# Performance work log

Hardware: AMD Instinct MI355X
Metric: run time of the kernel (lower is better)

Reference implementation:

```python
import jax, jax.numpy as jnp
import numpy as np

N, HW, L = 16, 3136, 64
C_IN, C_OUT, D = 256, 512, 256


def setup_inputs() -> dict:
    key = jax.random.key(0)
    ks = jax.random.split(key, 8)
    # xavier-normal-ish scale for weights
    def xav(k, shape):
        fan_in, fan_out = shape[1], shape[0]
        std = (2.0 / (fan_in + fan_out)) ** 0.5
        return jax.random.normal(k, shape, dtype=jnp.float32) * std
    return {
        "x": jax.random.normal(ks[0], (N, HW, C_IN), dtype=jnp.float32),
        "t": jax.random.normal(ks[1], (N, L, D), dtype=jnp.float32),
        "W1": xav(ks[2], (D, C_IN)),      # linear1 weight (out,in), no bias
        "W2": xav(ks[3], (D, D)),         # linear2 weight, no bias
        "W3": xav(ks[4], (C_OUT, D)),     # linear3 weight
        "b3": jnp.zeros((C_OUT,), dtype=jnp.float32),
        "Wd": xav(ks[5], (C_OUT, C_IN)),  # downsample weight
        "bd": jnp.zeros((C_OUT,), dtype=jnp.float32),
    }


def reference(x, t, W1, W2, W3, b3, Wd, bd):
    # x: (N, HW, C_in), t: (N, L, D)
    x_q = jnp.einsum("npc,dc->npd", x, W1)          # (N, HW, D)
    t_q = jnp.einsum("nld,ed->nle", t, W2)          # (N, L, D)
    a = jnp.einsum("npd,nld->npl", x_q, t_q)        # unscaled QK^T (N, HW, L)
    a = jax.nn.softmax(a, axis=2)
    t3 = jnp.einsum("nld,od->nlo", t, W3) + b3      # (N, L, C_out)
    av = jnp.einsum("npl,nlo->npo", a, t3)          # (N, HW, C_out)
    x_ds = jnp.einsum("npc,oc->npo", x, Wd) + bd    # downsample residual
    return x_ds + av
```

## Files before the change

kernel.cpp:

```cpp
#include <hip/hip_runtime.h>


typedef unsigned short u16;
using half8 = __attribute__((ext_vector_type(8))) _Float16;
using f32x4 = __attribute__((ext_vector_type(4))) float;

__device__ __forceinline__ u16 f2h(float f) {
  _Float16 h = (_Float16)f;
  union { _Float16 h; u16 u; } cv; cv.h = h;
  return cv.u;
}

__device__ __forceinline__ f32x4 mfma16(half8 a, half8 b, f32x4 c) {
  return __builtin_amdgcn_mfma_f32_16x16x32_f16(a, b, c, 0, 0, 0);
}

__global__ __launch_bounds__(256) void prep_kernel(
    const float* __restrict__ W1, const float* __restrict__ W2,
    const float* __restrict__ W3, const float* __restrict__ Wd,
    const float* __restrict__ t,
    u16* __restrict__ W3f, u16* __restrict__ Wdf, u16* __restrict__ tf,
    u16* __restrict__ Gtf) {
  int b = blockIdx.x, k = threadIdx.x;
  if (b < 2048) {
    const float* src; u16* dst; int row;
    if (b < 512)       { src = W3; dst = W3f; row = b; }
    else if (b < 1024) { src = Wd; dst = Wdf; row = b - 512; }
    else               { src = t;  dst = tf;  row = b - 1024; }
    float v = src[(size_t)row*256 + k];
    int flat = ((row >> 4)*8 + (k >> 5))*512 + ((k >> 3) & 3)*128 + (row & 15)*8 + (k & 7);
    dst[flat] = f2h(v);
  } else {
    int c = b - 2048;
    float g = 0.f;
    #pragma unroll 16
    for (int d = 0; d < 256; ++d)
      g = fmaf(W1[d*256 + c], W2[d*256 + k], g);
    int flat = ((c >> 4)*8 + (k >> 5))*512 + ((k >> 3) & 3)*128 + (c & 15)*8 + (k & 7);
    Gtf[flat] = f2h(g);
  }
}

__global__ __launch_bounds__(256) void mt_t3_kernel(
    const u16* __restrict__ tf, const u16* __restrict__ Gtf,
    const u16* __restrict__ W3f, const float* __restrict__ b3,
    u16* __restrict__ mtf, u16* __restrict__ t3f) {
  const int tid = threadIdx.x, w = tid >> 6, lane = tid & 63;
  const int quad = lane >> 4, l16 = lane & 15;
  const int b = blockIdx.x;

  if (b < 64) {
    const int n = b >> 2, eb = b & 3;
    const int gc = eb*4 + w;
    f32x4 acc[4];
    #pragma unroll
    for (int mt = 0; mt < 4; ++mt) acc[mt] = (f32x4){0.f, 0.f, 0.f, 0.f};
    #pragma unroll
    for (int kc = 0; kc < 8; ++kc) {
      half8 bf = *(const half8*)(Gtf + (gc*8 + kc)*512 + lane*8);
      #pragma unroll
      for (int mt = 0; mt < 4; ++mt) {
        half8 a = *(const half8*)(tf + ((n*4 + mt)*8 + kc)*512 + lane*8);
        acc[mt] = mfma16(a, bf, acc[mt]);
      }
    }
    #pragma unroll
    for (int mt = 0; mt < 4; ++mt)
      #pragma unroll
      for (int r = 0; r < 4; ++r) {
        int flat = ((n*4 + mt)*8 + eb*2 + (w >> 1))*512
                 + ((w & 1)*2 + (l16 >> 3))*128 + (quad*4 + r)*8 + (l16 & 7);
        mtf[flat] = f2h(acc[mt][r]);
      }
  } else {
    const int b2 = b - 64;
    const int n = b2 >> 3, ob = b2 & 7;
    const int gW3 = ob*4 + w;
    f32x4 acc[4];
    #pragma unroll
    for (int nt = 0; nt < 4; ++nt) acc[nt] = (f32x4){0.f, 0.f, 0.f, 0.f};
    #pragma unroll
    for (int kc = 0; kc < 8; ++kc) {
      half8 a = *(const half8*)(W3f + (gW3*8 + kc)*512 + lane*8);
      #pragma unroll
      for (int nt = 0; nt < 4; ++nt) {
        half8 bf = *(const half8*)(tf + ((n*4 + nt)*8 + kc)*512 + lane*8);
        acc[nt] = mfma16(a, bf, acc[nt]);
      }
    }
    #pragma unroll
    for (int nt = 0; nt < 4; ++nt)
      #pragma unroll
      for (int r = 0; r < 4; ++r) {
        int o = ob*64 + w*16 + quad*4 + r;
        int flat = ((n*32 + ob*4 + w)*2 + (nt >> 1))*512
                 + ((nt & 1)*2 + (l16 >> 3))*128 + (quad*4 + r)*8 + (l16 & 7);
        t3f[flat] = f2h(acc[nt][r] + b3[o]);
      }
  }
}

__global__ __launch_bounds__(512, 4) void main_kernel(
    const float* __restrict__ x, const u16* __restrict__ Wdf,
    const u16* __restrict__ mtf, const u16* __restrict__ t3f,
    const float* __restrict__ bd, float* __restrict__ out) {
  __shared__ __attribute__((aligned(16))) char smem[62464];
  u16* xs = (u16*)smem;
  u16* aw = (u16*)(smem + 33792);
  float* parts = (float*)(smem + 43008);
  float* scb = (float*)(smem + 44032);

  const int bid = blockIdx.x;
  const int n  = bid / 49;
  const int pt = bid - n*49;
  const int m0 = pt * 64;
  const int tid = threadIdx.x, w = tid >> 6, lane = tid & 63;
  const int quad = lane >> 4, l16 = lane & 15;
  const int rg = w & 3;
  const int lp = w >> 2;

  float bias[4];
  #pragma unroll
  for (int ot = 0; ot < 4; ++ot) bias[ot] = bd[w*64 + ot*16 + l16];

  {
    const float4* xg = (const float4*)(x + (size_t)(n*3136 + m0)*256);
    #pragma unroll
    for (int it = 0; it < 8; ++it) {
      int idx = it*512 + tid;
      int r = idx >> 6, c4 = idx & 63;
      float4 v = xg[idx];
      ushort4 u;
      u.x = f2h(v.x); u.y = f2h(v.y); u.z = f2h(v.z); u.w = f2h(v.w);
      *(ushort4*)(&xs[r*264 + c4*4]) = u;
    }
  }
  __syncthreads();

  f32x4 acc2[2];
  acc2[0] = (f32x4){0.f, 0.f, 0.f, 0.f};
  acc2[1] = (f32x4){0.f, 0.f, 0.f, 0.f};
  #pragma unroll
  for (int kc = 0; kc < 8; ++kc) {
    half8 a = *(const half8*)(&xs[(rg*16 + l16)*264 + kc*32 + quad*8]);
    #pragma unroll
    for (int j = 0; j < 2; ++j) {
      half8 bf = *(const half8*)(mtf + ((size_t)(n*4 + lp*2 + j)*8 + kc)*512 + lane*8);
      acc2[j] = mfma16(a, bf, acc2[j]);
    }
  }

  float mx_[4], ps_[4], e0_[4], e1_[4];
  #pragma unroll
  for (int r = 0; r < 4; ++r) {
    float s0 = acc2[0][r], s1 = acc2[1][r];
    float mx = fmaxf(s0, s1);
    #pragma unroll
    for (int off = 8; off >= 1; off >>= 1) mx = fmaxf(mx, __shfl_xor(mx, off, 64));
    float e0 = __expf(s0 - mx), e1 = __expf(s1 - mx);
    float ps = e0 + e1;
    #pragma unroll
    for (int off = 8; off >= 1; off >>= 1) ps += __shfl_xor(ps, off, 64);
    mx_[r] = mx; ps_[r] = ps; e0_[r] = e0; e1_[r] = e1;
    if (l16 == 0) {
      int row = rg*16 + quad*4 + r;
      parts[(row*2 + lp)*2]     = mx;
      parts[(row*2 + lp)*2 + 1] = ps;
    }
  }
  __syncthreads();

  #pragma unroll
  for (int r = 0; r < 4; ++r) {
    int row = rg*16 + quad*4 + r;
    float mxo = parts[(row*2 + (1 - lp))*2];
    float pso = parts[(row*2 + (1 - lp))*2 + 1];
    float g  = fmaxf(mx_[r], mxo);
    float sA = __expf(mx_[r] - g), sB = __expf(mxo - g);
    float inv = 1.0f / (ps_[r]*sA + pso*sB);
    float scl = sA * inv;
    aw[row*72 + (lp*2)*16 + l16]     = f2h(e0_[r]*scl);
    aw[row*72 + (lp*2 + 1)*16 + l16] = f2h(e1_[r]*scl);
  }
  __syncthreads();

  float* sc = scb + w*576;
  f32x4 acc[4][2];

  #pragma unroll
  for (int mt = 0; mt < 4; ++mt)
    #pragma unroll
    for (int ot = 0; ot < 2; ++ot) acc[mt][ot] = (f32x4){0.f, 0.f, 0.f, 0.f};
  #pragma unroll
  for (int kc = 0; kc < 8; ++kc) {
    half8 a[4];
    #pragma unroll
    for (int mt = 0; mt < 4; ++mt)
      a[mt] = *(const half8*)(&xs[(mt*16 + l16)*264 + kc*32 + quad*8]);
    #pragma unroll
    for (int ot = 0; ot < 2; ++ot) {
      half8 bf = *(const half8*)(Wdf + ((size_t)(w*4 + ot)*8 + kc)*512 + lane*8);
      #pragma unroll
      for (int mt = 0; mt < 4; ++mt) acc[mt][ot] = mfma16(a[mt], bf, acc[mt][ot]);
    }
  }
  #pragma unroll
  for (int kc3 = 0; kc3 < 2; ++kc3) {
    half8 a3[4];
    #pragma unroll
    for (int mt = 0; mt < 4; ++mt)
      a3[mt] = *(const half8*)(&aw[(mt*16 + l16)*72 + kc3*32 + quad*8]);
    #pragma unroll
    for (int ot = 0; ot < 2; ++ot) {
      half8 bf = *(const half8*)(t3f + ((size_t)(n*32 + w*4 + ot)*2 + kc3)*512 + lane*8);
      #pragma unroll
      for (int mt = 0; mt < 4; ++mt) acc[mt][ot] = mfma16(a3[mt], bf, acc[mt][ot]);
    }
  }
  #pragma unroll
  for (int mt = 0; mt < 4; ++mt) {
    #pragma unroll
    for (int ot = 0; ot < 2; ++ot)
      #pragma unroll
      for (int r = 0; r < 4; ++r)
        sc[(quad*4 + r)*36 + ot*16 + l16] = acc[mt][ot][r] + bias[ot];
    #pragma unroll
    for (int shot = 0; shot < 2; ++shot) {
      int row = shot*8 + (lane >> 3);
      float4 v = *(float4*)&sc[row*36 + (lane & 7)*4];
      *(float4*)&out[(size_t)(n*3136 + m0 + mt*16 + row)*512 + w*64 + (lane & 7)*4] = v;
    }
  }

  #pragma unroll
  for (int mt = 0; mt < 4; ++mt)
    #pragma unroll
    for (int ot = 0; ot < 2; ++ot) acc[mt][ot] = (f32x4){0.f, 0.f, 0.f, 0.f};
  #pragma unroll
  for (int kc = 0; kc < 8; ++kc) {
    half8 a[4];
    #pragma unroll
    for (int mt = 0; mt < 4; ++mt)
      a[mt] = *(const half8*)(&xs[(mt*16 + l16)*264 + kc*32 + quad*8]);
    #pragma unroll
    for (int ot = 0; ot < 2; ++ot) {
      half8 bf = *(const half8*)(Wdf + ((size_t)(w*4 + 2 + ot)*8 + kc)*512 + lane*8);
      #pragma unroll
      for (int mt = 0; mt < 4; ++mt) acc[mt][ot] = mfma16(a[mt], bf, acc[mt][ot]);
    }
  }
  #pragma unroll
  for (int kc3 = 0; kc3 < 2; ++kc3) {
    half8 a3[4];
    #pragma unroll
    for (int mt = 0; mt < 4; ++mt)
      a3[mt] = *(const half8*)(&aw[(mt*16 + l16)*72 + kc3*32 + quad*8]);
    #pragma unroll
    for (int ot = 0; ot < 2; ++ot) {
      half8 bf = *(const half8*)(t3f + ((size_t)(n*32 + w*4 + 2 + ot)*2 + kc3)*512 + lane*8);
      #pragma unroll
      for (int mt = 0; mt < 4; ++mt) acc[mt][ot] = mfma16(a3[mt], bf, acc[mt][ot]);
    }
  }
  #pragma unroll
  for (int mt = 0; mt < 4; ++mt) {
    #pragma unroll
    for (int ot = 0; ot < 2; ++ot)
      #pragma unroll
      for (int r = 0; r < 4; ++r)
        sc[(quad*4 + r)*36 + ot*16 + l16] = acc[mt][ot][r] + bias[2 + ot];
    #pragma unroll
    for (int shot = 0; shot < 2; ++shot) {
      int row = shot*8 + (lane >> 3);
      float4 v = *(float4*)&sc[row*36 + (lane & 7)*4];
      *(float4*)&out[(size_t)(n*3136 + m0 + mt*16 + row)*512 + w*64 + 32 + (lane & 7)*4] = v;
    }
  }
}

extern "C" void kernel_launch(void* const* d_in, const int* in_sizes, int n_in,
                              void* d_out, int out_size, void* d_ws, size_t ws_size,
                              hipStream_t stream) {
  const float* x  = (const float*)d_in[0];
  const float* t  = (const float*)d_in[1];
  const float* W1 = (const float*)d_in[2];
  const float* W2 = (const float*)d_in[3];
  const float* W3 = (const float*)d_in[4];
  const float* b3 = (const float*)d_in[5];
  const float* Wd = (const float*)d_in[6];
  const float* bd = (const float*)d_in[7];
  float* out = (float*)d_out;

  char* ws = (char*)d_ws;
  u16* W3f = (u16*)(ws + 0);
  u16* Wdf = (u16*)(ws + 262144);
  u16* tf  = (u16*)(ws + 524288);
  u16* Gtf = (u16*)(ws + 1048576);
  u16* mtf = (u16*)(ws + 1179648);
  u16* t3f = (u16*)(ws + 1703936);

  hipLaunchKernelGGL(prep_kernel, dim3(2304), dim3(256), 0, stream,
                     W1, W2, W3, Wd, t, W3f, Wdf, tf, Gtf);
  hipLaunchKernelGGL(mt_t3_kernel, dim3(192), dim3(256), 0, stream,
                     tf, Gtf, W3f, b3, mtf, t3f);
  hipLaunchKernelGGL(main_kernel, dim3(784), dim3(512), 0, stream,
                     x, Wdf, mtf, t3f, bd, out);
}
```

Baseline: 203.0 us.

## Make main kernel persistent with double-buffered x tile prefetch

The main kernel becomes persistent: it launches 256 blocks, one per CU, and each block loops over 3 or 4 of the 784 tiles. The next tile's x is loaded into registers early and converted into a second LDS buffer at the end of each iteration, so global loads overlap with MFMA work. This removes the wave-quantization tail and the per-block prologue. In exchange the LDS footprint grows, occupancy drops to 2 blocks per SM in launch bounds, and the 32 prefetch registers raise register pressure.

```diff
diff --git a/kernel.cpp b/kernel.cpp
--- a/kernel.cpp
+++ b/kernel.cpp
@@ -100,20 +100,19 @@
   }
 }
 
-__global__ __launch_bounds__(512, 4) void main_kernel(
+__global__ __launch_bounds__(512, 2) void main_kernel(
     const float* __restrict__ x, const u16* __restrict__ Wdf,
     const u16* __restrict__ mtf, const u16* __restrict__ t3f,
     const float* __restrict__ bd, float* __restrict__ out) {
-  __shared__ __attribute__((aligned(16))) char smem[62464];
-  u16* xs = (u16*)smem;
-  u16* aw = (u16*)(smem + 33792);
-  float* parts = (float*)(smem + 43008);
-  float* scb = (float*)(smem + 44032);
-
-  const int bid = blockIdx.x;
-  const int n  = bid / 49;
-  const int pt = bid - n*49;
-  const int m0 = pt * 64;
+  __shared__ __attribute__((aligned(16))) char smem[96256];
+  u16* xs0 = (u16*)smem;
+  u16* xs1 = (u16*)(smem + 33792);
+  u16* aw  = (u16*)(smem + 67584);
+  float* parts = (float*)(smem + 76800);
+  float* scb = (float*)(smem + 77824);
+
+  const int b = blockIdx.x;
+  const int NT = (b < 16) ? 4 : 3;
   const int tid = threadIdx.x, w = tid >> 6, lane = tid & 63;
   const int quad = lane >> 4, l16 = lane & 15;
   const int rg = w & 3;
@@ -123,158 +122,193 @@
   #pragma unroll
   for (int ot = 0; ot < 4; ++ot) bias[ot] = bd[w*64 + ot*16 + l16];
 
+  float* sc = scb + w*576;
+
+  float4 vx[8];
   {
-    const float4* xg = (const float4*)(x + (size_t)(n*3136 + m0)*256);
+    int n0 = b / 49, m00 = (b - n0*49)*64;
+    const float4* xg = (const float4*)(x + (size_t)(n0*3136 + m00)*256);
+    #pragma unroll
+    for (int it = 0; it < 8; ++it) vx[it] = xg[it*512 + tid];
     #pragma unroll
     for (int it = 0; it < 8; ++it) {
       int idx = it*512 + tid;
       int r = idx >> 6, c4 = idx & 63;
-      float4 v = xg[idx];
       ushort4 u;
-      u.x = f2h(v.x); u.y = f2h(v.y); u.z = f2h(v.z); u.w = f2h(v.w);
-      *(ushort4*)(&xs[r*264 + c4*4]) = u;
+      u.x = f2h(vx[it].x); u.y = f2h(vx[it].y);
+      u.z = f2h(vx[it].z); u.w = f2h(vx[it].w);
+      *(ushort4*)(&xs0[r*264 + c4*4]) = u;
     }
   }
   __syncthreads();
 
-  f32x4 acc2[2];
-  acc2[0] = (f32x4){0.f, 0.f, 0.f, 0.f};
-  acc2[1] = (f32x4){0.f, 0.f, 0.f, 0.f};
-  #pragma unroll
-  for (int kc = 0; kc < 8; ++kc) {
-    half8 a = *(const half8*)(&xs[(rg*16 + l16)*264 + kc*32 + quad*8]);
-    #pragma unroll
-    for (int j = 0; j < 2; ++j) {
-      half8 bf = *(const half8*)(mtf + ((size_t)(n*4 + lp*2 + j)*8 + kc)*512 + lane*8);
-      acc2[j] = mfma16(a, bf, acc2[j]);
-    }
-  }
-
-  float mx_[4], ps_[4], e0_[4], e1_[4];
-  #pragma unroll
-  for (int r = 0; r < 4; ++r) {
-    float s0 = acc2[0][r], s1 = acc2[1][r];
-    float mx = fmaxf(s0, s1);
-    #pragma unroll
-    for (int off = 8; off >= 1; off >>= 1) mx = fmaxf(mx, __shfl_xor(mx, off, 64));
-    float e0 = __expf(s0 - mx), e1 = __expf(s1 - mx);
-    float ps = e0 + e1;
-    #pragma unroll
-    for (int off = 8; off >= 1; off >>= 1) ps += __shfl_xor(ps, off, 64);
-    mx_[r] = mx; ps_[r] = ps; e0_[r] = e0; e1_[r] = e1;
-    if (l16 == 0) {
+  for (int ti = 0; ti < NT; ++ti) {
+    u16* xc = (ti & 1) ? xs1 : xs0;
+    u16* xn = (ti & 1) ? xs0 : xs1;
+    const int tile = b + ti*256;
+    const int n = tile / 49;
+    const int m0 = (tile - n*49)*64;
+    const bool more = (ti + 1 < NT);
+
+    if (more) {
+      int tile2 = b + (ti + 1)*256;
+      int n2 = tile2 / 49, m02 = (tile2 - n2*49)*64;
+      const float4* xg2 = (const float4*)(x + (size_t)(n2*3136 + m02)*256);
+      #pragma unroll
+      for (int it = 0; it < 8; ++it) vx[it] = xg2[it*512 + tid];
+    }
+
+    f32x4 acc2[2];
+    acc2[0] = (f32x4){0.f, 0.f, 0.f, 0.f};
+    acc2[1] = (f32x4){0.f, 0.f, 0.f, 0.f};
+    #pragma unroll
+    for (int kc = 0; kc < 8; ++kc) {
+      half8 a = *(const half8*)(&xc[(rg*16 + l16)*264 + kc*32 + quad*8]);
+      #pragma unroll
+      for (int j = 0; j < 2; ++j) {
+        half8 bf = *(const half8*)(mtf + ((size_t)(n*4 + lp*2 + j)*8 + kc)*512 + lane*8);
+        acc2[j] = mfma16(a, bf, acc2[j]);
+      }
+    }
+
+    float mx_[4], ps_[4], e0_[4], e1_[4];
+    #pragma unroll
+    for (int r = 0; r < 4; ++r) {
+      float s0 = acc2[0][r], s1 = acc2[1][r];
+      float mx = fmaxf(s0, s1);
+      #pragma unroll
+      for (int off = 8; off >= 1; off >>= 1) mx = fmaxf(mx, __shfl_xor(mx, off, 64));
+      float e0 = __expf(s0 - mx), e1 = __expf(s1 - mx);
+      float ps = e0 + e1;
+      #pragma unroll
+      for (int off = 8; off >= 1; off >>= 1) ps += __shfl_xor(ps, off, 64);
+      mx_[r] = mx; ps_[r] = ps; e0_[r] = e0; e1_[r] = e1;
+      if (l16 == 0) {
+        int row = rg*16 + quad*4 + r;
+        parts[(row*2 + lp)*2]     = mx;
+        parts[(row*2 + lp)*2 + 1] = ps;
+      }
+    }
+    __syncthreads();
+
+    #pragma unroll
+    for (int r = 0; r < 4; ++r) {
       int row = rg*16 + quad*4 + r;
-      parts[(row*2 + lp)*2]     = mx;
-      parts[(row*2 + lp)*2 + 1] = ps;
-    }
-  }
-  __syncthreads();
-
-  #pragma unroll
-  for (int r = 0; r < 4; ++r) {
-    int row = rg*16 + quad*4 + r;
-    float mxo = parts[(row*2 + (1 - lp))*2];
-    float pso = parts[(row*2 + (1 - lp))*2 + 1];
-    float g  = fmaxf(mx_[r], mxo);
-    float sA = __expf(mx_[r] - g), sB = __expf(mxo - g);
-    float inv = 1.0f / (ps_[r]*sA + pso*sB);
-    float scl = sA * inv;
-    aw[row*72 + (lp*2)*16 + l16]     = f2h(e0_[r]*scl);
-    aw[row*72 + (lp*2 + 1)*16 + l16] = f2h(e1_[r]*scl);
-  }
-  __syncthreads();
-
-  float* sc = scb + w*576;
-  f32x4 acc[4][2];
-
-  #pragma unroll
-  for (int mt = 0; mt < 4; ++mt)
-    #pragma unroll
-    for (int ot = 0; ot < 2; ++ot) acc[mt][ot] = (f32x4){0.f, 0.f, 0.f, 0.f};
-  #pragma unroll
-  for (int kc = 0; kc < 8; ++kc) {
-    half8 a[4];
+      float mxo = parts[(row*2 + (1 - lp))*2];
+      float pso = parts[(row*2 + (1 - lp))*2 + 1];
+      float g  = fmaxf(mx_[r], mxo);
+      float sA = __expf(mx_[r] - g), sB = __expf(mxo - g);
+      float inv = 1.0f / (ps_[r]*sA + pso*sB);
+      float scl = sA * inv;
+      aw[row*72 + (lp*2)*16 + l16]     = f2h(e0_[r]*scl);
+      aw[row*72 + (lp*2 + 1)*16 + l16] = f2h(e1_[r]*scl);
+    }
+    __syncthreads();
+
+    f32x4 acc[4][2];
+
     #pragma unroll
     for (int mt = 0; mt < 4; ++mt)
-      a[mt] = *(const half8*)(&xs[(mt*16 + l16)*264 + kc*32 + quad*8]);
-    #pragma unroll
-    for (int ot = 0; ot < 2; ++ot) {
-      half8 bf = *(const half8*)(Wdf + ((size_t)(w*4 + ot)*8 + kc)*512 + lane*8);
-      #pragma unroll
-      for (int mt = 0; mt < 4; ++mt) acc[mt][ot] = mfma16(a[mt], bf, acc[mt][ot]);
-    }
-  }
-  #pragma unroll
-  for (int kc3 = 0; kc3 < 2; ++kc3) {
-    half8 a3[4];
+      #pragma unroll
+      for (int ot = 0; ot < 2; ++ot) acc[mt][ot] = (f32x4){0.f, 0.f, 0.f, 0.f};
+    #pragma unroll
+    for (int kc = 0; kc < 8; ++kc) {
+      half8 a[4];
+      #pragma unroll
+      for (int mt = 0; mt < 4; ++mt)
+        a[mt] = *(const half8*)(&xc[(mt*16 + l16)*264 + kc*32 + quad*8]);
+      #pragma unroll
+      for (int ot = 0; ot < 2; ++ot) {
+        half8 bf = *(const half8*)(Wdf + ((size_t)(w*4 + ot)*8 + kc)*512 + lane*8);
+        #pragma unroll
+        for (int mt = 0; mt < 4; ++mt) acc[mt][ot] = mfma16(a[mt], bf, acc[mt][ot]);
+      }
+    }
+    #pragma unroll
+    for (int kc3 = 0; kc3 < 2; ++kc3) {
+      half8 a3[4];
+      #pragma unroll
+      for (int mt = 0; mt < 4; ++mt)
+        a3[mt] = *(const half8*)(&aw[(mt*16 + l16)*72 + kc3*32 + quad*8]);
+      #pragma unroll
+      for (int ot = 0; ot < 2; ++ot) {
+        half8 bf = *(const half8*)(t3f + ((size_t)(n*32 + w*4 + ot)*2 + kc3)*512 + lane*8);
+        #pragma unroll
+        for (int mt = 0; mt < 4; ++mt) acc[mt][ot] = mfma16(a3[mt], bf, acc[mt][ot]);
+      }
+    }
+    #pragma unroll
+    for (int mt = 0; mt < 4; ++mt) {
+      #pragma unroll
+      for (int ot = 0; ot < 2; ++ot)
+        #pragma unroll
+        for (int r = 0; r < 4; ++r)
+          sc[(quad*4 + r)*36 + ot*16 + l16] = acc[mt][ot][r] + bias[ot];
+      #pragma unroll
+      for (int shot = 0; shot < 2; ++shot) {
+        int row = shot*8 + (lane >> 3);
+        float4 v = *(float4*)&sc[row*36 + (lane & 7)*4];
+        *(float4*)&out[(size_t)(n*3136 + m0 + mt*16 + row)*512 + w*64 + (lane & 7)*4] = v;
+      }
+    }
+
     #pragma unroll
     for (int mt = 0; mt < 4; ++mt)
-      a3[mt] = *(const half8*)(&aw[(mt*16 + l16)*72 + kc3*32 + quad*8]);
-    #pragma unroll
-    for (int ot = 0; ot < 2; ++ot) {
-      half8 bf = *(const half8*)(t3f + ((size_t)(n*32 + w*4 + ot)*2 + kc3)*512 + lane*8);
-      #pragma unroll
-      for (int mt = 0; mt < 4; ++mt) acc[mt][ot] = mfma16(a3[mt], bf, acc[mt][ot]);
-    }
-  }
-  #pragma unroll
-  for (int mt = 0; mt < 4; ++mt) {
-    #pragma unroll
-    for (int ot = 0; ot < 2; ++ot)
-      #pragma unroll
-      for (int r = 0; r < 4; ++r)
-        sc[(quad*4 + r)*36 + ot*16 + l16] = acc[mt][ot][r] + bias[ot];
-    #pragma unroll
-    for (int shot = 0; shot < 2; ++shot) {
-      int row = shot*8 + (lane >> 3);
-      float4 v = *(float4*)&sc[row*36 + (lane & 7)*4];
-      *(float4*)&out[(size_t)(n*3136 + m0 + mt*16 + row)*512 + w*64 + (lane & 7)*4] = v;
-    }
-  }
-
-  #pragma unroll
-  for (int mt = 0; mt < 4; ++mt)
-    #pragma unroll
-    for (int ot = 0; ot < 2; ++ot) acc[mt][ot] = (f32x4){0.f, 0.f, 0.f, 0.f};
-  #pragma unroll
-  for (int kc = 0; kc < 8; ++kc) {
-    half8 a[4];
-    #pragma unroll
-    for (int mt = 0; mt < 4; ++mt)
-      a[mt] = *(const half8*)(&xs[(mt*16 + l16)*264 + kc*32 + quad*8]);
-    #pragma unroll
-    for (int ot = 0; ot < 2; ++ot) {
-      half8 bf = *(const half8*)(Wdf + ((size_t)(w*4 + 2 + ot)*8 + kc)*512 + lane*8);
-      #pragma unroll
-      for (int mt = 0; mt < 4; ++mt) acc[mt][ot] = mfma16(a[mt], bf, acc[mt][ot]);
-    }
-  }
-  #pragma unroll
-  for (int kc3 = 0; kc3 < 2; ++kc3) {
-    half8 a3[4];
-    #pragma unroll
-    for (int mt = 0; mt < 4; ++mt)
-      a3[mt] = *(const half8*)(&aw[(mt*16 + l16)*72 + kc3*32 + quad*8]);
-    #pragma unroll
-    for (int ot = 0; ot < 2; ++ot) {
-      half8 bf = *(const half8*)(t3f + ((size_t)(n*32 + w*4 + 2 + ot)*2 + kc3)*512 + lane*8);
-      #pragma unroll
-      for (int mt = 0; mt < 4; ++mt) acc[mt][ot] = mfma16(a3[mt], bf, acc[mt][ot]);
-    }
-  }
-  #pragma unroll
-  for (int mt = 0; mt < 4; ++mt) {
-    #pragma unroll
-    for (int ot = 0; ot < 2; ++ot)
-      #pragma unroll
-      for (int r = 0; r < 4; ++r)
-        sc[(quad*4 + r)*36 + ot*16 + l16] = acc[mt][ot][r] + bias[2 + ot];
-    #pragma unroll
-    for (int shot = 0; shot < 2; ++shot) {
-      int row = shot*8 + (lane >> 3);
-      float4 v = *(float4*)&sc[row*36 + (lane & 7)*4];
-      *(float4*)&out[(size_t)(n*3136 + m0 + mt*16 + row)*512 + w*64 + 32 + (lane & 7)*4] = v;
-    }
+      #pragma unroll
+      for (int ot = 0; ot < 2; ++ot) acc[mt][ot] = (f32x4){0.f, 0.f, 0.f, 0.f};
+    #pragma unroll
+    for (int kc = 0; kc < 8; ++kc) {
+      half8 a[4];
+      #pragma unroll
+      for (int mt = 0; mt < 4; ++mt)
+        a[mt] = *(const half8*)(&xc[(mt*16 + l16)*264 + kc*32 + quad*8]);
+      #pragma unroll
+      for (int ot = 0; ot < 2; ++ot) {
+        half8 bf = *(const half8*)(Wdf + ((size_t)(w*4 + 2 + ot)*8 + kc)*512 + lane*8);
+        #pragma unroll
+        for (int mt = 0; mt < 4; ++mt) acc[mt][ot] = mfma16(a[mt], bf, acc[mt][ot]);
+      }
+    }
+    #pragma unroll
+    for (int kc3 = 0; kc3 < 2; ++kc3) {
+      half8 a3[4];
+      #pragma unroll
+      for (int mt = 0; mt < 4; ++mt)
+        a3[mt] = *(const half8*)(&aw[(mt*16 + l16)*72 + kc3*32 + quad*8]);
+      #pragma unroll
+      for (int ot = 0; ot < 2; ++ot) {
+        half8 bf = *(const half8*)(t3f + ((size_t)(n*32 + w*4 + 2 + ot)*2 + kc3)*512 + lane*8);
+        #pragma unroll
+        for (int mt = 0; mt < 4; ++mt) acc[mt][ot] = mfma16(a3[mt], bf, acc[mt][ot]);
+      }
+    }
+    #pragma unroll
+    for (int mt = 0; mt < 4; ++mt) {
+      #pragma unroll
+      for (int ot = 0; ot < 2; ++ot)
+        #pragma unroll
+        for (int r = 0; r < 4; ++r)
+          sc[(quad*4 + r)*36 + ot*16 + l16] = acc[mt][ot][r] + bias[2 + ot];
+      #pragma unroll
+      for (int shot = 0; shot < 2; ++shot) {
+        int row = shot*8 + (lane >> 3);
+        float4 v = *(float4*)&sc[row*36 + (lane & 7)*4];
+        *(float4*)&out[(size_t)(n*3136 + m0 + mt*16 + row)*512 + w*64 + 32 + (lane & 7)*4] = v;
+      }
+    }
+
+    if (more) {
+      #pragma unroll
+      for (int it = 0; it < 8; ++it) {
+        int idx = it*512 + tid;
+        int r = idx >> 6, c4 = idx & 63;
+        ushort4 u;
+        u.x = f2h(vx[it].x); u.y = f2h(vx[it].y);
+        u.z = f2h(vx[it].z); u.w = f2h(vx[it].w);
+        *(ushort4*)(&xn[r*264 + c4*4]) = u;
+      }
+    }
+    __syncthreads();
   }
 }
 
@@ -303,6 +337,6 @@
                      W1, W2, W3, Wd, t, W3f, Wdf, tf, Gtf);
   hipLaunchKernelGGL(mt_t3_kernel, dim3(192), dim3(256), 0, stream,
                      tf, Gtf, W3f, b3, mtf, t3f);
-  hipLaunchKernelGGL(main_kernel, dim3(784), dim3(512), 0, stream,
+  hipLaunchKernelGGL(main_kernel, dim3(256), dim3(512), 0, stream,
                      x, Wdf, mtf, t3f, bd, out);
 }
```

Result: slower. 239.5 us (+18.0%).
